# Kernel optimization log

Hardware: AMD Instinct MI355X
Metric: run time of the kernel (lower is better)

Reference implementation:

```python
import jax, jax.numpy as jnp
import numpy as np

DX = 8e-6      # pixel pitch (m)
Z = 0.05       # propagation distance (m)
B, C, H, W = 8, 3, 1024, 1024


def setup_inputs() -> dict:
    key = jax.random.key(0)
    k1, k2 = jax.random.split(key)
    x_real = jax.random.normal(k1, (B, C, H, W), dtype=jnp.float32)
    x_imag = jax.random.normal(k2, (B, C, H, W), dtype=jnp.float32)
    wavelengths = jnp.asarray([450e-9, 532e-9, 632.8e-9], dtype=jnp.float32)
    return {"x_real": x_real, "x_imag": x_imag, "wavelengths": wavelengths}


def _transfer_function(wavelengths, h, w, dx, z):
    # Angular-spectrum transfer function per wavelength: [C, H, W] complex64
    fx = jnp.fft.fftfreq(w, d=dx).astype(jnp.float32)  # [W]
    fy = jnp.fft.fftfreq(h, d=dx).astype(jnp.float32)  # [H]
    f2 = fy[:, None] ** 2 + fx[None, :] ** 2           # [H, W]
    lam = wavelengths[:, None, None]                   # [C, 1, 1]
    arg = 1.0 - (lam ** 2) * f2[None]                  # [C, H, W]
    kz = (2.0 * jnp.pi / lam) * z * jnp.sqrt(jnp.maximum(arg, 0.0))
    Hc = jnp.exp(1j * kz.astype(jnp.complex64))
    # zero out evanescent components
    return jnp.where(arg > 0.0, Hc, jnp.zeros((), dtype=jnp.complex64))


def reference(x_real, x_imag, wavelengths):
    # Batched angular-spectrum propagation, one wavelength per channel.
    x = (x_real + 1j * x_imag).astype(jnp.complex64)   # [B, C, H, W]
    Hc = _transfer_function(wavelengths, H, W, DX, Z)  # [C, H, W]
    Xf = jnp.fft.fft2(x, axes=(-2, -1))
    out = jnp.fft.ifft2(Xf * Hc[None], axes=(-2, -1))  # [B, C, H, W] complex
    # return real/imag stacked so output is a float tensor: [2, B, C, H, W]
    return jnp.stack([out.real.astype(jnp.float32), out.imag.astype(jnp.float32)], axis=0)
```

## Files before the change

kernel.cpp:

```cpp
#include <hip/hip_runtime.h>
#include <math.h>


#define NIMG 24

static __device__ __forceinline__ void cmulf(float& ar, float& ai, float br, float bi) {
    float r = ar * br - ai * bi;
    float i = ar * bi + ai * br;
    ar = r; ai = i;
}

__device__ __forceinline__ float2 cadd(float2 a, float2 b){ return make_float2(a.x+b.x, a.y+b.y); }
__device__ __forceinline__ float2 csub(float2 a, float2 b){ return make_float2(a.x-b.x, a.y-b.y); }
__device__ __forceinline__ float2 cmul(float2 a, float c, float s){ return make_float2(a.x*c - a.y*s, a.x*s + a.y*c); }

__device__ __forceinline__ float2 computeH(float lam, int ky, int kx) {
    int iy = (ky < 512) ? ky : ky - 1024;
    int ix = (kx < 512) ? kx : kx - 1024;
    const double recip = 1.0 / (1024.0 * 8e-06);
    float fy = (float)((double)iy * recip);
    float fx = (float)((double)ix * recip);
    float f2  = __fadd_rn(__fmul_rn(fy, fy), __fmul_rn(fx, fx));
    float l2  = __fmul_rn(lam, lam);
    float arg = __fsub_rn(1.0f, __fmul_rn(l2, f2));
    float2 h = make_float2(0.0f, 0.0f);
    if (arg > 0.0f) {
        float t  = __fdiv_rn(6.28318530717958647692f, lam);
        t        = __fmul_rn(t, 0.05f);
        float kz = __fmul_rn(t, __fsqrt_rn(arg));
        double s, c;
        sincos((double)kz, &s, &c);
        const float sc = 9.5367431640625e-07f;
        h = make_float2((float)c * sc, (float)s * sc);
    }
    return h;
}

__global__ __launch_bounds__(256) void build_H(float2* __restrict__ Htab,
                                               const float* __restrict__ wl) {
    int idx = blockIdx.x * 256 + threadIdx.x;
    int c   = idx >> 20;
    int rem = idx & 1048575;
    Htab[idx] = computeH(wl[c], rem >> 10, rem & 1023);
}

template<int SIGN>
__device__ __forceinline__ void dft4nt(float2& a0, float2& a1, float2& a2, float2& a3) {
    float2 t0 = cadd(a0, a2), t1 = csub(a0, a2);
    float2 t2 = cadd(a1, a3), t3 = csub(a1, a3);
    a0 = cadd(t0, t2);
    a2 = csub(t0, t2);
    a1 = make_float2(t1.x - SIGN * t3.y, t1.y + SIGN * t3.x);
    a3 = make_float2(t1.x + SIGN * t3.y, t1.y - SIGN * t3.x);
}

template<int SIGN>
__device__ __forceinline__ void dft4(float2& a0, float2& a1, float2& a2, float2& a3,
                                     float c1, float s1) {
    float c2 = c1*c1 - s1*s1, s2 = 2.f*c1*s1;
    float c3 = c2*c1 - s2*s1, s3 = s2*c1 + c2*s1;
    a1 = cmul(a1, c1, s1);
    a2 = cmul(a2, c2, s2);
    a3 = cmul(a3, c3, s3);
    dft4nt<SIGN>(a0, a1, a2, a3);
}

template<int SIGN>
__device__ __forceinline__ void fft_line(float* re, float* im, int j) {
    #pragma unroll
    for (int s = 0; s < 5; ++s) {
        const int Ns = 1 << (2 * s);
        const int jm = j & (Ns - 1);
        float ang = (float)(SIGN * jm) * (3.14159265358979323846f / (2.0f * (float)Ns));
        float c1, s1; __sincosf(ang, &s1, &c1);
        float c2 = c1 * c1 - s1 * s1, s2 = 2.0f * c1 * s1;
        float c3 = c2 * c1 - s2 * s1, s3 = s2 * c1 + c2 * s1;
        float ar[4], ai[4];
        #pragma unroll
        for (int r = 0; r < 4; ++r) { ar[r] = re[j + (r << 8)]; ai[r] = im[j + (r << 8)]; }
        cmulf(ar[1], ai[1], c1, s1);
        cmulf(ar[2], ai[2], c2, s2);
        cmulf(ar[3], ai[3], c3, s3);
        float t0r = ar[0] + ar[2], t0i = ai[0] + ai[2];
        float t1r = ar[0] - ar[2], t1i = ai[0] - ai[2];
        float t2r = ar[1] + ar[3], t2i = ai[1] + ai[3];
        float t3r = ar[1] - ar[3], t3i = ai[1] - ai[3];
        float X0r = t0r + t2r, X0i = t0i + t2i;
        float X2r = t0r - t2r, X2i = t0i - t2i;
        float X1r = t1r - SIGN * t3i, X1i = t1i + SIGN * t3r;
        float X3r = t1r + SIGN * t3i, X3i = t1i - SIGN * t3r;
        __syncthreads();
        const int jd = ((j >> (2 * s)) << (2 * s + 2)) + jm;
        re[jd] = X0r;            im[jd] = X0i;
        re[jd + Ns] = X1r;       im[jd + Ns] = X1i;
        re[jd + 2 * Ns] = X2r;   im[jd + 2 * Ns] = X2i;
        re[jd + 3 * Ns] = X3r;   im[jd + 3 * Ns] = X3i;
        __syncthreads();
    }
}

__global__ __launch_bounds__(256) void fft_rows_fwd(const float* __restrict__ xr,
                                                    const float* __restrict__ xi,
                                                    float2* __restrict__ out) {
    __shared__ float re[1024], im[1024];
    const int j = threadIdx.x;
    const long long base = (long long)blockIdx.x * 1024;
    const float4* r4 = (const float4*)(xr + base);
    const float4* i4 = (const float4*)(xi + base);
    float4 a = r4[j], b = i4[j];
    re[4 * j + 0] = a.x; re[4 * j + 1] = a.y; re[4 * j + 2] = a.z; re[4 * j + 3] = a.w;
    im[4 * j + 0] = b.x; im[4 * j + 1] = b.y; im[4 * j + 2] = b.z; im[4 * j + 3] = b.w;
    __syncthreads();
    fft_line<-1>(re, im, j);
    float4* o4 = (float4*)(out + base);
    o4[2 * j + 0] = make_float4(re[4 * j + 0], im[4 * j + 0], re[4 * j + 1], im[4 * j + 1]);
    o4[2 * j + 1] = make_float4(re[4 * j + 2], im[4 * j + 2], re[4 * j + 3], im[4 * j + 3]);
}

__global__ __launch_bounds__(256) void ifft_rows_out(const float2* __restrict__ in,
                                                     float* __restrict__ outr,
                                                     float* __restrict__ outi) {
    __shared__ float re[1024], im[1024];
    const int j = threadIdx.x;
    const long long base = (long long)blockIdx.x * 1024;
    const float4* in4 = (const float4*)(in + base);
    float4 a = in4[2 * j + 0], b = in4[2 * j + 1];
    re[4 * j + 0] = a.x; im[4 * j + 0] = a.y;
    re[4 * j + 1] = a.z; im[4 * j + 1] = a.w;
    re[4 * j + 2] = b.x; im[4 * j + 2] = b.y;
    re[4 * j + 3] = b.z; im[4 * j + 3] = b.w;
    __syncthreads();
    fft_line<1>(re, im, j);
    float4* or4 = (float4*)(outr + base);
    float4* oi4 = (float4*)(outi + base);
    or4[j] = make_float4(re[4 * j + 0], re[4 * j + 1], re[4 * j + 2], re[4 * j + 3]);
    oi4[j] = make_float4(im[4 * j + 0], im[4 * j + 1], im[4 * j + 2], im[4 * j + 3]);
}


#define WSYNC() do { asm volatile("s_waitcnt lgkmcnt(0)" ::: "memory"); \
                     __builtin_amdgcn_wave_barrier(); } while (0)

template<int SIGN>
__device__ __forceinline__ void wave_fft(char* cb, int l) {
    const float SPI8   = SIGN * 0.39269908169872415481f;
    const float SPI32  = SIGN * 0.09817477042468103870f;
    const float SPI128 = SIGN * 0.02454369260617025967f;
    const float SPI512 = SIGN * 0.00613592315154256492f;
    const int swzE = (((l >> 4)    ) & 7) << 4;
    const int swzO = (((l >> 4) + 4) & 7) << 4;
    char* rbE = cb + ((8 * l) ^ swzE);
    char* rbO = cb + ((8 * l) ^ swzO);
    float2 v[4][4];

    #pragma unroll
    for (int k = 0; k < 4; ++k) {
        #pragma unroll
        for (int r = 0; r < 4; ++r) {
            const int tt = k + 4 * r;
            v[k][r] = *(const float2*)(((tt & 1) ? rbO : rbE) + 512 * tt);
        }
    }
    #pragma unroll
    for (int k = 0; k < 4; ++k) dft4nt<SIGN>(v[k][0], v[k][1], v[k][2], v[k][3]);
    dft4nt<SIGN>(v[0][0], v[1][0], v[2][0], v[3][0]);
    #pragma unroll
    for (int q = 1; q < 4; ++q) {
        float s1, c1; __sincosf((float)q * SPI8, &s1, &c1);
        dft4<SIGN>(v[0][q], v[1][q], v[2][q], v[3][q], c1, s1);
    }
    {
        char* wb = cb + 128 * l;
        const int L7 = l & 7;
        #pragma unroll
        for (int p = 0; p < 4; ++p) {
            *(float4*)(wb + 16 * ((2*p+0) ^ L7)) =
                make_float4(v[p][0].x, v[p][0].y, v[p][1].x, v[p][1].y);
            *(float4*)(wb + 16 * ((2*p+1) ^ L7)) =
                make_float4(v[p][2].x, v[p][2].y, v[p][3].x, v[p][3].y);
        }
    }
    WSYNC();

    #pragma unroll
    for (int k = 0; k < 4; ++k) {
        #pragma unroll
        for (int r = 0; r < 4; ++r) {
            const int tt = k + 4 * r;
            v[k][r] = *(const float2*)(((tt & 1) ? rbO : rbE) + 512 * tt);
        }
    }
    {
        const int jm2 = l & 15;
        float s1, c1; __sincosf((float)jm2 * SPI32, &s1, &c1);
        #pragma unroll
        for (int k = 0; k < 4; ++k) dft4<SIGN>(v[k][0], v[k][1], v[k][2], v[k][3], c1, s1);
        const int lo8 = 8 * (l & 15);
        const int hi  = 2048 * (l >> 4);
        #pragma unroll
        for (int q = 0; q < 4; ++q) {
            float s1b, c1b; __sincosf((float)(jm2 + 16 * q) * SPI128, &s1b, &c1b);
            dft4<SIGN>(v[0][q], v[1][q], v[2][q], v[3][q], c1b, s1b);
            #pragma unroll
            for (int p = 0; p < 4; ++p) {
                const int K = ((q + 4 * p) & 7) << 4;
                *(float2*)(cb + (lo8 ^ K) + hi + 128 * q + 512 * p) = v[p][q];
            }
        }
    }
    WSYNC();

    #pragma unroll
    for (int m = 0; m < 4; ++m) {
        #pragma unroll
        for (int r = 0; r < 4; ++r) {
            const int tt = m + 4 * r;
            v[m][r] = *(const float2*)(((tt & 1) ? rbO : rbE) + 512 * tt);
        }
    }
    #pragma unroll
    for (int m = 0; m < 4; ++m) {
        float s1, c1; __sincosf((float)(l + 64 * m) * SPI512, &s1, &c1);
        dft4<SIGN>(v[m][0], v[m][1], v[m][2], v[m][3], c1, s1);
        #pragma unroll
        for (int q = 0; q < 4; ++q) {
            const int tt = m + 4 * q;
            *(float2*)(((tt & 1) ? rbO : rbE) + 512 * tt) = v[m][q];
        }
    }
}

__global__ __launch_bounds__(512, 4) void fft_cols_H(float2* __restrict__ ws,
                                                     const float2* __restrict__ Htab,
                                                     const float* __restrict__ wl) {
    __shared__ float4 ldsb[4096];
    char* lds = (char*)ldsb;
    const int t   = threadIdx.x;
    const int img = blockIdx.x >> 7;
    const int x0  = (blockIdx.x & 127) << 3;
    const int lamIdx = img % 3;
    const long long ibase = (long long)img << 20;

    const int c2  = t & 3;
    const int row = t >> 2;
    const int xr  = (8 * row) ^ (((row >> 4) & 7) << 4);
    char* io0 = lds + 16384 * c2 + xr;
    char* io1 = io0 + 8192;

    {
        const float2* src = ws + ibase + x0 + 2 * c2;
        #pragma unroll
        for (int k = 0; k < 8; ++k) {
            int y = row + 128 * k;
            float4 g = *(const float4*)(src + (long long)y * 1024);
            *(float2*)(io0 + 1024 * k) = make_float2(g.x, g.y);
            *(float2*)(io1 + 1024 * k) = make_float2(g.z, g.w);
        }
    }
    __syncthreads();

    const int w = t >> 6, l = t & 63;
    char* cb = lds + 8192 * w;
    wave_fft<-1>(cb, l);
    __syncthreads();

    {
        const float2* hsrc = Htab ? (Htab + (((long long)lamIdx) << 20) + x0 + 2 * c2)
                                  : nullptr;
        #pragma unroll
        for (int k = 0; k < 8; ++k) {
            int ky = row + 128 * k;
            float2 h0, h1;
            if (hsrc) {
                float4 hh = *(const float4*)(hsrc + (long long)ky * 1024);
                h0 = make_float2(hh.x, hh.y); h1 = make_float2(hh.z, hh.w);
            } else {
                h0 = computeH(wl[lamIdx], ky, x0 + 2 * c2);
                h1 = computeH(wl[lamIdx], ky, x0 + 2 * c2 + 1);
            }
            float2* p0 = (float2*)(io0 + 1024 * k);
            float2* p1 = (float2*)(io1 + 1024 * k);
            float2 a = *p0;
            *p0 = make_float2(a.x * h0.x - a.y * h0.y, a.x * h0.y + a.y * h0.x);
            float2 b = *p1;
            *p1 = make_float2(b.x * h1.x - b.y * h1.y, b.x * h1.y + b.y * h1.x);
        }
    }
    __syncthreads();

    wave_fft<1>(cb, l);
    __syncthreads();

    {
        float2* dst = ws + ibase + x0 + 2 * c2;
        #pragma unroll
        for (int k = 0; k < 8; ++k) {
            int y = row + 128 * k;
            float2 a = *(const float2*)(io0 + 1024 * k);
            float2 b = *(const float2*)(io1 + 1024 * k);
            *(float4*)(dst + (long long)y * 1024) = make_float4(a.x, a.y, b.x, b.y);
        }
    }
}

extern "C" void kernel_launch(void* const* d_in, const int* in_sizes, int n_in,
                              void* d_out, int out_size, void* d_ws, size_t ws_size,
                              hipStream_t stream) {
    const float* xr = (const float*)d_in[0];
    const float* xi = (const float*)d_in[1];
    const float* wl = (const float*)d_in[2];
    float* out = (float*)d_out;

    const size_t planeElems = (size_t)NIMG * 1024 * 1024;
    float2* wsC = (float2*)d_ws;
    const size_t needC = planeElems * sizeof(float2);
    const size_t needH = (size_t)3 * 1024 * 1024 * sizeof(float2);
    float2* Htab = nullptr;
    if (ws_size >= needC + needH) {
        Htab = (float2*)((char*)d_ws + needC);
        build_H<<<12288, 256, 0, stream>>>(Htab, wl);
    }
    fft_rows_fwd<<<NIMG * 1024, 256, 0, stream>>>(xr, xi, wsC);
    fft_cols_H<<<NIMG * 128, 512, 0, stream>>>(wsC, Htab, wl);
    ifft_rows_out<<<NIMG * 1024, 256, 0, stream>>>(wsC, out, out + planeElems);
}
```

Measured before the change: 319.7 us.

## Transpose intermediate so column FFTs read contiguous rows, using wave FFT everywhere

Replaces the block-level row FFTs, which synced the whole block at every radix-4 stage, with the per-wave register/LDS FFT in all three passes. The forward row pass now writes its result transposed into the workspace, so the second pass handles each column as a contiguous row with one wave per line and no block barriers. The transfer-function table is also built transposed to match. The final inverse row pass reads the transposed data back in 8-row groups and writes planar real and imaginary outputs. This trades strided column access for transposed scatter/gather writes and reads in the first and last passes.

```diff
diff --git a/kernel.cpp b/kernel.cpp
--- a/kernel.cpp
+++ b/kernel.cpp
@@ -9,10 +9,14 @@
     float i = ar * bi + ai * br;
     ar = r; ai = i;
 }
-
 __device__ __forceinline__ float2 cadd(float2 a, float2 b){ return make_float2(a.x+b.x, a.y+b.y); }
 __device__ __forceinline__ float2 csub(float2 a, float2 b){ return make_float2(a.x-b.x, a.y-b.y); }
 __device__ __forceinline__ float2 cmul(float2 a, float c, float s){ return make_float2(a.x*c - a.y*s, a.x*s + a.y*c); }
+
+__device__ __forceinline__ int SW(int j) {
+    int b = j << 3;
+    return b ^ (((b >> 7) & 7) << 4);
+}
 
 __device__ __forceinline__ float2 computeH(float lam, int ky, int kx) {
     int iy = (ky < 512) ? ky : ky - 1024;
@@ -36,12 +40,12 @@
     return h;
 }
 
-__global__ __launch_bounds__(256) void build_H(float2* __restrict__ Htab,
-                                               const float* __restrict__ wl) {
+__global__ __launch_bounds__(256) void build_H_T(float2* __restrict__ Htab,
+                                                 const float* __restrict__ wl) {
     int idx = blockIdx.x * 256 + threadIdx.x;
     int c   = idx >> 20;
     int rem = idx & 1048575;
-    Htab[idx] = computeH(wl[c], rem >> 10, rem & 1023);
+    Htab[idx] = computeH(wl[c], rem & 1023, rem >> 10);
 }
 
 template<int SIGN>
@@ -53,7 +57,6 @@
     a1 = make_float2(t1.x - SIGN * t3.y, t1.y + SIGN * t3.x);
     a3 = make_float2(t1.x + SIGN * t3.y, t1.y - SIGN * t3.x);
 }
-
 template<int SIGN>
 __device__ __forceinline__ void dft4(float2& a0, float2& a1, float2& a2, float2& a3,
                                      float c1, float s1) {
@@ -64,79 +67,6 @@
     a3 = cmul(a3, c3, s3);
     dft4nt<SIGN>(a0, a1, a2, a3);
 }
-
-template<int SIGN>
-__device__ __forceinline__ void fft_line(float* re, float* im, int j) {
-    #pragma unroll
-    for (int s = 0; s < 5; ++s) {
-        const int Ns = 1 << (2 * s);
-        const int jm = j & (Ns - 1);
-        float ang = (float)(SIGN * jm) * (3.14159265358979323846f / (2.0f * (float)Ns));
-        float c1, s1; __sincosf(ang, &s1, &c1);
-        float c2 = c1 * c1 - s1 * s1, s2 = 2.0f * c1 * s1;
-        float c3 = c2 * c1 - s2 * s1, s3 = s2 * c1 + c2 * s1;
-        float ar[4], ai[4];
-        #pragma unroll
-        for (int r = 0; r < 4; ++r) { ar[r] = re[j + (r << 8)]; ai[r] = im[j + (r << 8)]; }
-        cmulf(ar[1], ai[1], c1, s1);
-        cmulf(ar[2], ai[2], c2, s2);
-        cmulf(ar[3], ai[3], c3, s3);
-        float t0r = ar[0] + ar[2], t0i = ai[0] + ai[2];
-        float t1r = ar[0] - ar[2], t1i = ai[0] - ai[2];
-        float t2r = ar[1] + ar[3], t2i = ai[1] + ai[3];
-        float t3r = ar[1] - ar[3], t3i = ai[1] - ai[3];
-        float X0r = t0r + t2r, X0i = t0i + t2i;
-        float X2r = t0r - t2r, X2i = t0i - t2i;
-        float X1r = t1r - SIGN * t3i, X1i = t1i + SIGN * t3r;
-        float X3r = t1r + SIGN * t3i, X3i = t1i - SIGN * t3r;
-        __syncthreads();
-        const int jd = ((j >> (2 * s)) << (2 * s + 2)) + jm;
-        re[jd] = X0r;            im[jd] = X0i;
-        re[jd + Ns] = X1r;       im[jd + Ns] = X1i;
-        re[jd + 2 * Ns] = X2r;   im[jd + 2 * Ns] = X2i;
-        re[jd + 3 * Ns] = X3r;   im[jd + 3 * Ns] = X3i;
-        __syncthreads();
-    }
-}
-
-__global__ __launch_bounds__(256) void fft_rows_fwd(const float* __restrict__ xr,
-                                                    const float* __restrict__ xi,
-                                                    float2* __restrict__ out) {
-    __shared__ float re[1024], im[1024];
-    const int j = threadIdx.x;
-    const long long base = (long long)blockIdx.x * 1024;
-    const float4* r4 = (const float4*)(xr + base);
-    const float4* i4 = (const float4*)(xi + base);
-    float4 a = r4[j], b = i4[j];
-    re[4 * j + 0] = a.x; re[4 * j + 1] = a.y; re[4 * j + 2] = a.z; re[4 * j + 3] = a.w;
-    im[4 * j + 0] = b.x; im[4 * j + 1] = b.y; im[4 * j + 2] = b.z; im[4 * j + 3] = b.w;
-    __syncthreads();
-    fft_line<-1>(re, im, j);
-    float4* o4 = (float4*)(out + base);
-    o4[2 * j + 0] = make_float4(re[4 * j + 0], im[4 * j + 0], re[4 * j + 1], im[4 * j + 1]);
-    o4[2 * j + 1] = make_float4(re[4 * j + 2], im[4 * j + 2], re[4 * j + 3], im[4 * j + 3]);
-}
-
-__global__ __launch_bounds__(256) void ifft_rows_out(const float2* __restrict__ in,
-                                                     float* __restrict__ outr,
-                                                     float* __restrict__ outi) {
-    __shared__ float re[1024], im[1024];
-    const int j = threadIdx.x;
-    const long long base = (long long)blockIdx.x * 1024;
-    const float4* in4 = (const float4*)(in + base);
-    float4 a = in4[2 * j + 0], b = in4[2 * j + 1];
-    re[4 * j + 0] = a.x; im[4 * j + 0] = a.y;
-    re[4 * j + 1] = a.z; im[4 * j + 1] = a.w;
-    re[4 * j + 2] = b.x; im[4 * j + 2] = b.y;
-    re[4 * j + 3] = b.z; im[4 * j + 3] = b.w;
-    __syncthreads();
-    fft_line<1>(re, im, j);
-    float4* or4 = (float4*)(outr + base);
-    float4* oi4 = (float4*)(outi + base);
-    or4[j] = make_float4(re[4 * j + 0], re[4 * j + 1], re[4 * j + 2], re[4 * j + 3]);
-    oi4[j] = make_float4(im[4 * j + 0], im[4 * j + 1], im[4 * j + 2], im[4 * j + 3]);
-}
-
 
 #define WSYNC() do { asm volatile("s_waitcnt lgkmcnt(0)" ::: "memory"); \
                      __builtin_amdgcn_wave_barrier(); } while (0)
@@ -230,76 +160,138 @@
     }
 }
 
-__global__ __launch_bounds__(512, 4) void fft_cols_H(float2* __restrict__ ws,
-                                                     const float2* __restrict__ Htab,
-                                                     const float* __restrict__ wl) {
+__global__ __launch_bounds__(512, 4) void k1_rows_T(const float* __restrict__ xr,
+                                                    const float* __restrict__ xi,
+                                                    float2* __restrict__ T) {
     __shared__ float4 ldsb[4096];
     char* lds = (char*)ldsb;
-    const int t   = threadIdx.x;
+    const int t = threadIdx.x, w = t >> 6, l = t & 63;
     const int img = blockIdx.x >> 7;
-    const int x0  = (blockIdx.x & 127) << 3;
-    const int lamIdx = img % 3;
-    const long long ibase = (long long)img << 20;
-
-    const int c2  = t & 3;
-    const int row = t >> 2;
-    const int xr  = (8 * row) ^ (((row >> 4) & 7) << 4);
-    char* io0 = lds + 16384 * c2 + xr;
-    char* io1 = io0 + 8192;
-
-    {
-        const float2* src = ws + ibase + x0 + 2 * c2;
-        #pragma unroll
-        for (int k = 0; k < 8; ++k) {
-            int y = row + 128 * k;
-            float4 g = *(const float4*)(src + (long long)y * 1024);
-            *(float2*)(io0 + 1024 * k) = make_float2(g.x, g.y);
-            *(float2*)(io1 + 1024 * k) = make_float2(g.z, g.w);
-        }
-    }
-    __syncthreads();
-
-    const int w = t >> 6, l = t & 63;
+    const int y0  = (blockIdx.x & 127) << 3;
+    const long long ib = (long long)img << 20;
     char* cb = lds + 8192 * w;
+
+    {
+        const float4* rr = (const float4*)(xr + ib + (long long)(y0 + w) * 1024);
+        const float4* ri = (const float4*)(xi + ib + (long long)(y0 + w) * 1024);
+        const int swz = ((l >> 2) & 7) << 4;
+        #pragma unroll
+        for (int k = 0; k < 4; ++k) {
+            float4 a = rr[64 * k + l], b = ri[64 * k + l];
+            *(float4*)(cb + 2048 * k + ((32 * l) ^ swz))      = make_float4(a.x, b.x, a.y, b.y);
+            *(float4*)(cb + 2048 * k + ((32 * l + 16) ^ swz)) = make_float4(a.z, b.z, a.w, b.w);
+        }
+    }
+    WSYNC();
     wave_fft<-1>(cb, l);
     __syncthreads();
 
     {
-        const float2* hsrc = Htab ? (Htab + (((long long)lamIdx) << 20) + x0 + 2 * c2)
+        const int seg = t & 3;
+        const int xb  = t >> 2;
+        #pragma unroll
+        for (int k = 0; k < 8; ++k) {
+            int x = xb + 128 * k;
+            float2 v0 = *(const float2*)(lds + 8192 * (2 * seg)     + SW(x));
+            float2 v1 = *(const float2*)(lds + 8192 * (2 * seg + 1) + SW(x));
+            *(float4*)(T + ib + (long long)x * 1024 + y0 + 2 * seg) =
+                make_float4(v0.x, v0.y, v1.x, v1.y);
+        }
+    }
+}
+
+__global__ __launch_bounds__(256, 4) void k2_cols_H(float2* __restrict__ T,
+                                                    const float2* __restrict__ Htab,
+                                                    const float* __restrict__ wl) {
+    __shared__ float4 ldsb[2048];
+    char* lds = (char*)ldsb;
+    const int t = threadIdx.x, w = t >> 6, l = t & 63;
+    const int img = blockIdx.x >> 8;
+    const int x   = ((blockIdx.x & 255) << 2) + w;
+    const int lamIdx = img % 3;
+    char* cb = lds + 8192 * w;
+    float2* row = T + ((long long)img << 20) + (long long)x * 1024;
+    const int swz = ((l >> 3) & 7) << 4;
+
+    #pragma unroll
+    for (int k = 0; k < 8; ++k) {
+        float4 g = ((const float4*)row)[64 * k + l];
+        *(float4*)(cb + 1024 * k + ((16 * l) ^ swz)) = g;
+    }
+    WSYNC();
+    wave_fft<-1>(cb, l);
+    WSYNC();
+    {
+        const float2* hrow = Htab ? (Htab + ((long long)lamIdx << 20) + (long long)x * 1024)
                                   : nullptr;
+        const float lam = Htab ? 0.0f : wl[lamIdx];
         #pragma unroll
         for (int k = 0; k < 8; ++k) {
-            int ky = row + 128 * k;
-            float2 h0, h1;
-            if (hsrc) {
-                float4 hh = *(const float4*)(hsrc + (long long)ky * 1024);
-                h0 = make_float2(hh.x, hh.y); h1 = make_float2(hh.z, hh.w);
+            float4* p = (float4*)(cb + 1024 * k + ((16 * l) ^ swz));
+            float4 a = *p;
+            float4 h;
+            if (hrow) {
+                h = ((const float4*)hrow)[64 * k + l];
             } else {
-                h0 = computeH(wl[lamIdx], ky, x0 + 2 * c2);
-                h1 = computeH(wl[lamIdx], ky, x0 + 2 * c2 + 1);
+                int m = 128 * k + 2 * l;
+                float2 h0 = computeH(lam, m,     x);
+                float2 h1 = computeH(lam, m + 1, x);
+                h = make_float4(h0.x, h0.y, h1.x, h1.y);
             }
-            float2* p0 = (float2*)(io0 + 1024 * k);
-            float2* p1 = (float2*)(io1 + 1024 * k);
-            float2 a = *p0;
-            *p0 = make_float2(a.x * h0.x - a.y * h0.y, a.x * h0.y + a.y * h0.x);
-            float2 b = *p1;
-            *p1 = make_float2(b.x * h1.x - b.y * h1.y, b.x * h1.y + b.y * h1.x);
-        }
-    }
-    __syncthreads();
-
+            *p = make_float4(a.x * h.x - a.y * h.y, a.x * h.y + a.y * h.x,
+                             a.z * h.z - a.w * h.w, a.z * h.w + a.w * h.z);
+        }
+    }
+    WSYNC();
     wave_fft<1>(cb, l);
-    __syncthreads();
-
-    {
-        float2* dst = ws + ibase + x0 + 2 * c2;
-        #pragma unroll
-        for (int k = 0; k < 8; ++k) {
-            int y = row + 128 * k;
-            float2 a = *(const float2*)(io0 + 1024 * k);
-            float2 b = *(const float2*)(io1 + 1024 * k);
-            *(float4*)(dst + (long long)y * 1024) = make_float4(a.x, a.y, b.x, b.y);
-        }
+    WSYNC();
+    #pragma unroll
+    for (int k = 0; k < 8; ++k) {
+        float4 g = *(const float4*)(cb + 1024 * k + ((16 * l) ^ swz));
+        ((float4*)row)[64 * k + l] = g;
+    }
+}
+
+__global__ __launch_bounds__(512, 4) void k3_irows_T(const float2* __restrict__ T,
+                                                     float* __restrict__ outr,
+                                                     float* __restrict__ outi) {
+    __shared__ float4 ldsb[4096];
+    char* lds = (char*)ldsb;
+    const int t = threadIdx.x, w = t >> 6, l = t & 63;
+    const int img = blockIdx.x >> 6;
+    const int y0  = (blockIdx.x & 63) << 4;
+    const long long ib = (long long)img << 20;
+    char* cb = lds + 8192 * w;
+
+    for (int p = 0; p < 2; ++p) {
+        const int yb = y0 + 8 * p;
+        {
+            const int seg = t & 3;
+            const int xb  = t >> 2;
+            #pragma unroll
+            for (int k = 0; k < 8; ++k) {
+                int x = xb + 128 * k;
+                float4 g = *(const float4*)(T + ib + (long long)x * 1024 + yb + 2 * seg);
+                *(float2*)(lds + 8192 * (2 * seg)     + SW(x)) = make_float2(g.x, g.y);
+                *(float2*)(lds + 8192 * (2 * seg + 1) + SW(x)) = make_float2(g.z, g.w);
+            }
+        }
+        __syncthreads();
+        wave_fft<1>(cb, l);
+        WSYNC();
+        {
+            float4* pr = (float4*)(outr + ib + (long long)(yb + w) * 1024);
+            float4* pi = (float4*)(outi + ib + (long long)(yb + w) * 1024);
+            const int swz = ((l >> 2) & 7) << 4;
+            #pragma unroll
+            for (int k = 0; k < 4; ++k) {
+                float4 c0 = *(const float4*)(cb + 2048 * k + ((32 * l) ^ swz));
+                float4 c1 = *(const float4*)(cb + 2048 * k + ((32 * l + 16) ^ swz));
+                pr[64 * k + l] = make_float4(c0.x, c0.z, c1.x, c1.z);
+                pi[64 * k + l] = make_float4(c0.y, c0.w, c1.y, c1.w);
+            }
+        }
+        __syncthreads();
     }
 }
 
@@ -318,9 +310,9 @@
     float2* Htab = nullptr;
     if (ws_size >= needC + needH) {
         Htab = (float2*)((char*)d_ws + needC);
-        build_H<<<12288, 256, 0, stream>>>(Htab, wl);
-    }
-    fft_rows_fwd<<<NIMG * 1024, 256, 0, stream>>>(xr, xi, wsC);
-    fft_cols_H<<<NIMG * 128, 512, 0, stream>>>(wsC, Htab, wl);
-    ifft_rows_out<<<NIMG * 1024, 256, 0, stream>>>(wsC, out, out + planeElems);
-}
+        build_H_T<<<12288, 256, 0, stream>>>(Htab, wl);
+    }
+    k1_rows_T<<<NIMG * 128, 512, 0, stream>>>(xr, xi, wsC);
+    k2_cols_H<<<NIMG * 256, 256, 0, stream>>>(wsC, Htab, wl);
+    k3_irows_T<<<NIMG * 64, 512, 0, stream>>>(wsC, out, out + planeElems);
+}
```

After: 470.4 us. +47.1%, slower.
